# Performance work log

Hardware: AMD Instinct MI355X
Metric: run time of the kernel (lower is better)

The kernel has to match this reference:

```python
import jax, jax.numpy as jnp
import numpy as np

T, H, W = 16, 48, 48
C2D, C3D, DIM = 64, 64, 6
EPS = 1e-5


def _centered(s):
    # torch.linspace(-0.5*(s-1), 0.5*(s-1), s) == arange(s) - (s-1)/2
    return jnp.arange(s, dtype=jnp.float32) - 0.5 * (s - 1)


def _g_vol(t, h, w):
    grids = jnp.meshgrid(_centered(t), _centered(h), _centered(w), indexing='ij')
    return jnp.stack(grids, axis=-1).reshape(-1, 3)  # (Vs, 3)


def _g_slice(h, w):
    grids = jnp.meshgrid(_centered(1), _centered(h), _centered(w), indexing='ij')
    return jnp.stack(grids, axis=1)  # (1, 3, H, W)


def _layernorm(x, gamma, beta):
    mu = jnp.mean(x, axis=-1, keepdims=True)
    var = jnp.mean(jnp.square(x - mu), axis=-1, keepdims=True)
    return (x - mu) * jax.lax.rsqrt(var + EPS) * gamma + beta


def setup_inputs() -> dict:
    key = jax.random.key(0)
    ks = jax.random.split(key, 4)
    vol = jax.random.normal(ks[0], (1, C3D, T, H, W), dtype=jnp.float32)
    slc = jax.random.normal(ks[1], (1, C2D, H, W), dtype=jnp.float32)
    # proj weights ~ Normal(0, 1e-5) as in the torch module; biases zero
    w2d = jax.random.normal(ks[2], (DIM, C2D), dtype=jnp.float32) * 1e-5
    w3d = jax.random.normal(ks[3], (DIM, C3D), dtype=jnp.float32) * 1e-5
    return {
        'vol': vol, 'slc': slc,
        'w2d': w2d, 'b2d': jnp.zeros((DIM,), jnp.float32),
        'g2d': jnp.ones((DIM,), jnp.float32), 'be2d': jnp.zeros((DIM,), jnp.float32),
        'w3d': w3d, 'b3d': jnp.zeros((DIM,), jnp.float32),
        'g3d': jnp.ones((DIM,), jnp.float32), 'be3d': jnp.zeros((DIM,), jnp.float32),
    }


def reference(vol, slc, w2d, b2d, g2d, be2d, w3d, b3d, g3d, be3d):
    B, C, t, h, w = vol.shape
    Vs, Ss = t * h * w, h * w
    # ProjectLN2D: permute -> linear -> LN; flatten spatial to tokens
    q = _layernorm(jnp.einsum('bchw,dc->bhwd', slc, w2d) + b2d, g2d, be2d).reshape(B, Ss, -1)
    k = _layernorm(jnp.einsum('bcthw,dc->bthwd', vol, w3d) + b3d, g3d, be3d).reshape(B, Vs, -1)
    attn = jax.nn.softmax(jnp.einsum('bsd,bvd->bsv', q, k), axis=-1)  # (B, Ss, Vs)
    g_pred = jnp.einsum('bsv,vx->bsx', attn, _g_vol(t, h, w))  # (B, Ss, 3)
    flow = jnp.transpose(g_pred, (0, 2, 1)).reshape(B, 3, h, w) - _g_slice(h, w)
    return flow
```

## Files before the change

### kernel.cpp

```cpp
#include <hip/hip_runtime.h>
#include <math.h>

#define TT 16
#define HH 48
#define WW 48
#define CC 64
#define DD 6
#define VS (TT*HH*WW)
#define SS (HH*WW)
#define NT (VS/16)
#define QW 64
#define NFR 4
#define NQG (SS/QW)
#define NCH 128
#define TPC (NT/NCH)
#define LOG2E 1.44269504088896f

typedef float  f4 __attribute__((ext_vector_type(4)));
typedef float  f2 __attribute__((ext_vector_type(2)));
typedef _Float16 h4 __attribute__((ext_vector_type(4)));
typedef _Float16 h2 __attribute__((ext_vector_type(2)));

__global__ __launch_bounds__(256) void proj_kernel(
    const float* __restrict__ vol, const float* __restrict__ slc,
    const float* __restrict__ w2d, const float* __restrict__ b2d,
    const float* __restrict__ g2d, const float* __restrict__ be2d,
    const float* __restrict__ w3d, const float* __restrict__ b3d,
    const float* __restrict__ g3d, const float* __restrict__ be3d,
    f4* __restrict__ Kf, float* __restrict__ Qp)
{
    int tid = threadIdx.x;
    int gid = blockIdx.x * 256 + tid;
    __shared__ float sk[256][7];

    bool isK = gid < VS;
    const float *src, *wgt, *bia, *gam, *bet;
    int pos, stride;
    if (isK) { src = vol; wgt = w3d; bia = b3d; gam = g3d; bet = be3d; pos = gid;      stride = VS; }
    else     { src = slc; wgt = w2d; bia = b2d; gam = g2d; bet = be2d; pos = gid - VS; stride = SS; }

    float y[DD];
    {
        float acc[DD] = {0.f,0.f,0.f,0.f,0.f,0.f};
        #pragma unroll
        for (int c = 0; c < CC; ++c) {
            float x = src[c * stride + pos];
            #pragma unroll
            for (int d = 0; d < DD; ++d) acc[d] = fmaf(wgt[d*CC + c], x, acc[d]);
        }
        float mu = 0.f;
        #pragma unroll
        for (int d = 0; d < DD; ++d) { acc[d] += bia[d]; mu += acc[d]; }
        mu *= (1.f/DD);
        float var = 0.f;
        #pragma unroll
        for (int d = 0; d < DD; ++d) { float t = acc[d] - mu; var = fmaf(t, t, var); }
        var *= (1.f/DD);
        float inv = rsqrtf(var + 1e-5f);
        #pragma unroll
        for (int d = 0; d < DD; ++d) y[d] = (acc[d] - mu) * inv * gam[d] + bet[d];
    }

    if (isK) {
        #pragma unroll
        for (int d = 0; d < DD; ++d) sk[tid][d] = y[d];
        __syncthreads();

        int tl = tid >> 4;
        int r  = tid & 15;
        int tileg = blockIdx.x * 16 + tl;
        #pragma unroll
        for (int g = 0; g < 4; ++g) {
            h4 kh = (h4){0,0,0,0};
            if (g == 0) {
                kh = (h4){ (_Float16)sk[tl*16+r][0], (_Float16)sk[tl*16+r][1],
                           (_Float16)sk[tl*16+r][2], (_Float16)sk[tl*16+r][3] };
            } else if (g == 1) {
                kh = (h4){ (_Float16)sk[tl*16+r][4], (_Float16)sk[tl*16+r][5],
                           (_Float16)0.f, (_Float16)0.f };
            }
            h4 gh = (h4){0,0,0,0};
            if (r < 4) {
                #pragma unroll
                for (int j = 0; j < 4; ++j) {
                    int v   = tileg*16 + g*4 + j;
                    int t   = v / (HH*WW);
                    int rem = v - t*(HH*WW);
                    int h   = rem / WW;
                    int w   = rem - h*WW;
                    float val = (r==0) ? (float)t - 7.5f
                              : (r==1) ? (float)h - 23.5f
                              : (r==2) ? (float)w - 23.5f
                              :          1.0f;
                    gh[j] = (_Float16)val;
                }
            }
            f2 kl = __builtin_bit_cast(f2, kh);
            f2 gl = __builtin_bit_cast(f2, gh);
            f4 o = (f4){kl.x, kl.y, gl.x, gl.y};
            Kf[tileg*64 + r + 16*g] = o;
        }
    } else {
        #pragma unroll
        for (int d = 0; d < DD; ++d) Qp[pos*8 + d] = y[d] * LOG2E;
        Qp[pos*8 + 6] = 0.f;
        Qp[pos*8 + 7] = 0.f;
    }
}

__global__ __launch_bounds__(64, 8) void attn_kernel(
    const f4* __restrict__ Kf, const float* __restrict__ Qp,
    float* __restrict__ Pc)
{
    int lane = threadIdx.x;
    int g = lane >> 4, r = lane & 15;
    int qg = blockIdx.x >> 7;
    int ch = blockIdx.x & (NCH-1);
    int qbase = qg*QW;

    h4 qf[NFR];
    #pragma unroll
    for (int f = 0; f < NFR; ++f) {
        qf[f] = (h4){0,0,0,0};
        if (g < 2) {
            f4 qv = *(const f4*)(Qp + (qbase + f*16 + r)*8 + g*4);
            qf[f] = (h4){ (_Float16)qv.x, (_Float16)qv.y, (_Float16)qv.z, (_Float16)qv.w };
        }
    }

    f4 z = (f4){0,0,0,0};
    f4 out[NFR];
    #pragma unroll
    for (int f = 0; f < NFR; ++f) out[f] = z;

    const f4* kp = Kf + (ch*TPC)*64 + lane;
    f4 v = kp[0];
    for (int it = 0; it < TPC; ++it) {
        f4 vn;
        if (it + 1 < TPC) vn = kp[(it+1)*64];
        h4 ka = __builtin_bit_cast(h4, (f2){v.x, v.y});
        h4 ga = __builtin_bit_cast(h4, (f2){v.z, v.w});
        #pragma unroll
        for (int f = 0; f < NFR; ++f) {
            f4 s = __builtin_amdgcn_mfma_f32_16x16x16f16(ka, qf[f], z, 0, 0, 0);
            float p0 = __builtin_amdgcn_exp2f(s.x);
            float p1 = __builtin_amdgcn_exp2f(s.y);
            float p2 = __builtin_amdgcn_exp2f(s.z);
            float p3 = __builtin_amdgcn_exp2f(s.w);
            h2 pl = __builtin_bit_cast(h2, __builtin_amdgcn_cvt_pkrtz(p0, p1));
            h2 ph = __builtin_bit_cast(h2, __builtin_amdgcn_cvt_pkrtz(p2, p3));
            h4 pf = (h4){pl.x, pl.y, ph.x, ph.y};
            out[f] = __builtin_amdgcn_mfma_f32_16x16x16f16(pf, ga, out[f], 0, 0, 0);
        }
        v = vn;
    }
    if (r < 4) {
        #pragma unroll
        for (int f = 0; f < NFR; ++f)
            #pragma unroll
            for (int j = 0; j < 4; ++j) {
                int q = qbase + f*16 + g*4 + j;
                Pc[(ch*SS + q)*4 + r] = out[f][j];
            }
    }
}

__global__ __launch_bounds__(256) void final_kernel(
    const f4* __restrict__ Pc, float* __restrict__ out)
{
    int q = blockIdx.x * 256 + threadIdx.x;
    if (q >= SS) return;
    f4 a = (f4){0,0,0,0};
    #pragma unroll 8
    for (int c = 0; c < NCH; ++c) a += Pc[c*SS + q];
    float inv = 1.f / a.w;
    int h = q / WW;
    int w = q - h*WW;
    out[q]        = a.x * inv;
    out[SS + q]   = a.y * inv - ((float)h - 23.5f);
    out[2*SS + q] = a.z * inv - ((float)w - 23.5f);
}

extern "C" void kernel_launch(void* const* d_in, const int* in_sizes, int n_in,
                              void* d_out, int out_size, void* d_ws, size_t ws_size,
                              hipStream_t stream)
{
    const float* vol  = (const float*)d_in[0];
    const float* slc  = (const float*)d_in[1];
    const float* w2d  = (const float*)d_in[2];
    const float* b2d  = (const float*)d_in[3];
    const float* g2d  = (const float*)d_in[4];
    const float* be2d = (const float*)d_in[5];
    const float* w3d  = (const float*)d_in[6];
    const float* b3d  = (const float*)d_in[7];
    const float* g3d  = (const float*)d_in[8];
    const float* be3d = (const float*)d_in[9];
    float* out = (float*)d_out;

    f4*    Kf = (f4*)d_ws;
    float* Qp = (float*)(Kf + NT*64);
    f4*    Pc = (f4*)(Qp + SS*8);

    proj_kernel<<<(VS + SS)/256, 256, 0, stream>>>(vol, slc, w2d, b2d, g2d, be2d,
                                                   w3d, b3d, g3d, be3d, Kf, Qp);
    attn_kernel<<<NQG*NCH, 64, 0, stream>>>(Kf, Qp, (float*)Pc);
    final_kernel<<<(SS + 255)/256, 256, 0, stream>>>(Pc, out);
}
```

Baseline: 36.40 us.

## Regroup attention into 4-wave blocks, double key chunks, transpose partials for wave reduction

The attention kernel now runs 256-thread blocks that cover four 64-query groups sharing the same key chunk. The number of key chunks doubles to 256, so each block does less serial work, and the per-chunk loop is fully unrolled. The partial sums are stored query-major so the final kernel can reduce each query with one wave using coalesced loads and shuffles. The trade-off is twice the partial-sum traffic and a larger reduction. The channel loop in the projection kernel is no longer force-unrolled.

```diff
diff --git a/kernel.cpp b/kernel.cpp
--- a/kernel.cpp
+++ b/kernel.cpp
@@ -9,10 +9,9 @@
 #define VS (TT*HH*WW)
 #define SS (HH*WW)
 #define NT (VS/16)
-#define QW 64
 #define NFR 4
-#define NQG (SS/QW)
-#define NCH 128
+#define NQB (SS/256)
+#define NCH 256
 #define TPC (NT/NCH)
 #define LOG2E 1.44269504088896f
 
@@ -42,7 +41,6 @@
     float y[DD];
     {
         float acc[DD] = {0.f,0.f,0.f,0.f,0.f,0.f};
-        #pragma unroll
         for (int c = 0; c < CC; ++c) {
             float x = src[c * stride + pos];
             #pragma unroll
@@ -108,15 +106,17 @@
     }
 }
 
-__global__ __launch_bounds__(64, 8) void attn_kernel(
+__global__ __launch_bounds__(256, 6) void attn_kernel(
     const f4* __restrict__ Kf, const float* __restrict__ Qp,
     float* __restrict__ Pc)
 {
-    int lane = threadIdx.x;
+    int tid  = threadIdx.x;
+    int wv   = tid >> 6;
+    int lane = tid & 63;
     int g = lane >> 4, r = lane & 15;
-    int qg = blockIdx.x >> 7;
+    int qb = blockIdx.x >> 8;
     int ch = blockIdx.x & (NCH-1);
-    int qbase = qg*QW;
+    int qbase = qb*256 + wv*64;
 
     h4 qf[NFR];
     #pragma unroll
@@ -135,6 +135,7 @@
 
     const f4* kp = Kf + (ch*TPC)*64 + lane;
     f4 v = kp[0];
+    #pragma unroll
     for (int it = 0; it < TPC; ++it) {
         f4 vn;
         if (it + 1 < TPC) vn = kp[(it+1)*64];
@@ -160,7 +161,7 @@
             #pragma unroll
             for (int j = 0; j < 4; ++j) {
                 int q = qbase + f*16 + g*4 + j;
-                Pc[(ch*SS + q)*4 + r] = out[f][j];
+                Pc[(q*NCH + ch)*4 + r] = out[f][j];
             }
     }
 }
@@ -168,17 +169,29 @@
 __global__ __launch_bounds__(256) void final_kernel(
     const f4* __restrict__ Pc, float* __restrict__ out)
 {
-    int q = blockIdx.x * 256 + threadIdx.x;
-    if (q >= SS) return;
+    int wv   = threadIdx.x >> 6;
+    int lane = threadIdx.x & 63;
+    int q = blockIdx.x * 4 + wv;
+
     f4 a = (f4){0,0,0,0};
-    #pragma unroll 8
-    for (int c = 0; c < NCH; ++c) a += Pc[c*SS + q];
-    float inv = 1.f / a.w;
-    int h = q / WW;
-    int w = q - h*WW;
-    out[q]        = a.x * inv;
-    out[SS + q]   = a.y * inv - ((float)h - 23.5f);
-    out[2*SS + q] = a.z * inv - ((float)w - 23.5f);
+    #pragma unroll
+    for (int i = 0; i < NCH/64; ++i) a += Pc[q*NCH + i*64 + lane];
+
+    #pragma unroll
+    for (int off = 32; off >= 1; off >>= 1) {
+        a.x += __shfl_xor(a.x, off);
+        a.y += __shfl_xor(a.y, off);
+        a.z += __shfl_xor(a.z, off);
+        a.w += __shfl_xor(a.w, off);
+    }
+    if (lane == 0) {
+        float inv = 1.f / a.w;
+        int h = q / WW;
+        int w = q - h*WW;
+        out[q]        = a.x * inv;
+        out[SS + q]   = a.y * inv - ((float)h - 23.5f);
+        out[2*SS + q] = a.z * inv - ((float)w - 23.5f);
+    }
 }
 
 extern "C" void kernel_launch(void* const* d_in, const int* in_sizes, int n_in,
@@ -203,6 +216,6 @@
 
     proj_kernel<<<(VS + SS)/256, 256, 0, stream>>>(vol, slc, w2d, b2d, g2d, be2d,
                                                    w3d, b3d, g3d, be3d, Kf, Qp);
-    attn_kernel<<<NQG*NCH, 64, 0, stream>>>(Kf, Qp, (float*)Pc);
-    final_kernel<<<(SS + 255)/256, 256, 0, stream>>>(Pc, out);
-}
+    attn_kernel<<<NQB*NCH, 256, 0, stream>>>(Kf, Qp, (float*)Pc);
+    final_kernel<<<SS/4, 256, 0, stream>>>(Pc, out);
+}
```

Result: faster. 33.65 us (-7.6%).
